# Performance work log

Hardware: AMD Instinct MI355X
Metric: run time of the kernel (lower is better)

The kernel has to match this reference:

```python
import jax, jax.numpy as jnp
import numpy as np

T, B_SZ = 1024, 1024
NX, NU, ND, NM, NDT, NH = 128, 64, 32, 32, 32, 128


def setup_inputs() -> dict:
    key = jax.random.key(0)
    ks = jax.random.split(key, 10)
    return {
        "x": jax.random.normal(ks[0], (B_SZ, NX), jnp.float32),
        "M_flow": jax.random.normal(ks[1], (T, B_SZ, NM), jnp.float32),
        "DT": jax.random.normal(ks[2], (T, B_SZ, NDT), jnp.float32),
        "D": jax.random.normal(ks[3], (T, B_SZ, ND), jnp.float32),
        # ConstrainedLinear(nx, nx): weight and scalar init with torch.rand -> uniform[0,1)
        "A_weight": jax.random.uniform(ks[4], (NX, NX), jnp.float32),
        "A_scalar": jax.random.uniform(ks[5], (NX, NX), jnp.float32),
        # nn.Linear(in, out, bias=False) weights are [out, in]
        "B_w": jax.random.normal(ks[6], (NX, NU), jnp.float32) * (1.0 / np.sqrt(NU)),
        "E_w": jax.random.normal(ks[7], (NX, ND), jnp.float32) * (1.0 / np.sqrt(ND)),
        "hf1_w": jax.random.normal(ks[8], (NH, NM + NDT), jnp.float32) * (1.0 / np.sqrt(NM + NDT)),
        "hf2_w": jax.random.normal(ks[9], (NU, NH), jnp.float32) * (1.0 / np.sqrt(NH)),
    }


def reference(x, M_flow, DT, D, A_weight, A_scalar, B_w, E_w, hf1_w, hf2_w):
    # Constrained weight: ((1 - 0.1*sigmoid(scalar)) * softmax(weight, dim=1)).T
    # It is constant across time, so compute once (torch redundantly recomputes it per step).
    s_clamped = 1.0 - 0.1 * jax.nn.sigmoid(A_scalar)
    W_eff = (s_clamped * jax.nn.softmax(A_weight, axis=1)).T  # [nx, nx]

    # Per-step control input u_t depends only on exogenous M_flow/DT -> vectorize over time.
    md = jnp.concatenate([M_flow, DT], axis=2)                # [T, B, n_m+n_dT]
    h = jax.nn.relu(jnp.einsum('tbi,hi->tbh', md, hf1_w))     # [T, B, n_hidden]
    u = jax.nn.relu(jnp.einsum('tbh,uh->tbu', h, hf2_w))      # [T, B, nu]

    # Precompute additive drive B(u_t) + E(d_t); only x@W_eff is sequential.
    drive = jnp.einsum('tbu,xu->tbx', u, B_w) + jnp.einsum('tbd,xd->tbx', D, E_w)

    def step(x_prev, drive_t):
        x_new = x_prev @ W_eff + drive_t
        return x_new, x_new

    _, X = jax.lax.scan(step, x, drive)  # X: [T, B, nx]
    Y = X[:, :, -1]                      # [T, B]
    return X, Y
```

## Files before the change

### kernel.cpp

```cpp
#include <hip/hip_runtime.h>

typedef _Float16 h4 __attribute__((ext_vector_type(4)));
typedef _Float16 h8 __attribute__((ext_vector_type(8)));
typedef float f4 __attribute__((ext_vector_type(4)));

#define MFMA16(a, b, c) __builtin_amdgcn_mfma_f32_16x16x32_f16((a), (b), (c), 0, 0, 0)

static constexpr int TT  = 1024;
static constexpr int BS  = 1024;
static constexpr int LCH = 64;
static constexpr int NCH = 16;
static constexpr size_t XTOT = (size_t)TT * BS * 128;

static constexpr size_t WS_WT16 = 0;
static constexpr size_t WS_HF1  = 32768;
static constexpr size_t WS_HF2  = 49152;
static constexpr size_t WS_BW   = 65536;
static constexpr size_t WS_EW   = 81920;
static constexpr size_t WS_WL16 = 90112;
static constexpr size_t WS_W32A = 122880;
static constexpr size_t WS_W32B = 188416;
static constexpr size_t WS_F    = 253952;
static constexpr size_t WS_INIT = WS_F + (size_t)16 * 1024 * 128 * 4;

__global__ void prep_kernel(const float* __restrict__ Aw, const float* __restrict__ As,
                            const float* __restrict__ hf1, const float* __restrict__ hf2,
                            const float* __restrict__ Bw, const float* __restrict__ Ew,
                            char* __restrict__ ws)
{
    const int tid = threadIdx.x;
    const int bid = blockIdx.x;
    if (bid < 128) {
        __shared__ float red[128];
        const int n = bid;
        const float a = Aw[n * 128 + tid];
        red[tid] = a;
        __syncthreads();
        for (int s = 64; s > 0; s >>= 1) {
            if (tid < s) red[tid] = fmaxf(red[tid], red[tid + s]);
            __syncthreads();
        }
        const float mx = red[0];
        __syncthreads();
        const float e = expf(a - mx);
        red[tid] = e;
        __syncthreads();
        for (int s = 64; s > 0; s >>= 1) {
            if (tid < s) red[tid] += red[tid + s];
            __syncthreads();
        }
        const float sm  = e / red[0];
        const float asv = As[n * 128 + tid];
        const float sc  = 1.0f - 0.1f * (1.0f / (1.0f + expf(-asv)));
        const float val = sc * sm;
        ((_Float16*)(ws + WS_WT16))[n * 128 + tid] = (_Float16)val;
        ((float*)(ws + WS_W32A))[n * 128 + tid]    = val;
    } else {
        const int b2 = bid - 128;
        for (int i = b2 * 128 + tid; i < 8192; i += 32 * 128) {
            ((_Float16*)(ws + WS_HF1))[i] = (_Float16)hf1[i];
            ((_Float16*)(ws + WS_HF2))[i] = (_Float16)hf2[i];
            ((_Float16*)(ws + WS_BW))[i]  = (_Float16)Bw[i];
            if (i < 4096) ((_Float16*)(ws + WS_EW))[i] = (_Float16)Ew[i];
        }
    }
}

__global__ void matsq_kernel(const float* __restrict__ in, float* __restrict__ out)
{
    const int idx = blockIdx.x * 256 + threadIdx.x;
    const int n = idx >> 7, k = idx & 127;
    float acc = 0.f;
    for (int m = 0; m < 128; ++m) acc += in[m * 128 + k] * in[n * 128 + m];
    out[idx] = acc;
}

__global__ void conv_kernel(const float* __restrict__ in, char* __restrict__ ws)
{
    const int idx = blockIdx.x * 256 + threadIdx.x;
    ((_Float16*)(ws + WS_WL16))[idx] = (_Float16)in[idx];
}

template <bool FINAL>
__global__ __launch_bounds__(256, 2)
void scan_chunk(const float* __restrict__ Mfl, const float* __restrict__ DTi,
                const float* __restrict__ Din, char* __restrict__ ws,
                float* __restrict__ Xout, float* __restrict__ Yout)
{
    const int tid  = threadIdx.x;
    const int lane = tid & 63;
    const int w    = tid >> 6;
    const int cl   = lane & 15;
    const int gq   = lane >> 4;
    const int bt   = blockIdx.x & 63;
    const int c    = blockIdx.x >> 6;
    const int b0   = bt * 16;

    const _Float16* Wt16 = (const _Float16*)(ws + WS_WT16);
    const _Float16* Hf1  = (const _Float16*)(ws + WS_HF1);
    const _Float16* Hf2  = (const _Float16*)(ws + WS_HF2);
    const _Float16* Bw16 = (const _Float16*)(ws + WS_BW);
    const _Float16* Ew16 = (const _Float16*)(ws + WS_EW);
    float* Fbuf          = (float*)(ws + WS_F);
    const float* Init    = (const float*)(ws + WS_INIT);

    __shared__ __align__(16) _Float16 xs[2][16 * 128];
    __shared__ __align__(16) _Float16 mds[16 * 64];
    __shared__ __align__(16) _Float16 hs[16 * 128];
    __shared__ __align__(16) _Float16 us[16 * 64];
    __shared__ __align__(16) _Float16 dts[16 * 32];

    h8 wtf[2][4], hf1f[2][2], bwf[2][2], ewf[2], hf2f[4];
#pragma unroll
    for (int nt = 0; nt < 2; ++nt) {
        const int ng = w * 32 + nt * 16 + cl;
#pragma unroll
        for (int kk = 0; kk < 4; ++kk)
            wtf[nt][kk] = *(const h8*)&Wt16[ng * 128 + kk * 32 + gq * 8];
#pragma unroll
        for (int kk = 0; kk < 2; ++kk) {
            hf1f[nt][kk] = *(const h8*)&Hf1[ng * 64 + kk * 32 + gq * 8];
            bwf[nt][kk]  = *(const h8*)&Bw16[ng * 64 + kk * 32 + gq * 8];
        }
        ewf[nt] = *(const h8*)&Ew16[ng * 32 + gq * 8];
    }
    {
        const int ng = w * 16 + cl;
#pragma unroll
        for (int kk = 0; kk < 4; ++kk)
            hf2f[kk] = *(const h8*)&Hf2[ng * 128 + kk * 32 + gq * 8];
    }

    if constexpr (FINAL) {
        const int row = tid >> 4, c8 = tid & 15;
        const float* src = &Init[((size_t)c * BS + b0 + row) * 128 + c8 * 8];
        f4 v0 = *(const f4*)src;
        f4 v1 = *(const f4*)(src + 4);
        h8 hv;
#pragma unroll
        for (int j = 0; j < 4; ++j) { hv[j] = (_Float16)v0[j]; hv[4 + j] = (_Float16)v1[j]; }
        *(h8*)&xs[0][row * 128 + ((c8 ^ row) & 15) * 8] = hv;
    } else {
        h8 z = {};
        *(h8*)&xs[0][tid * 8] = z;
    }

    f4 p0, p1;
    const int qrow = (tid & 127) >> 3;
    const int qc4  = (tid & 7) * 4;
    auto loadin = [&](int k) {
        const size_t t  = (size_t)c * LCH + k;
        const size_t rb = (t * BS + b0 + qrow) * 32 + qc4;
        p0 = (tid < 128) ? *(const f4*)&Mfl[rb] : *(const f4*)&DTi[rb];
        if (tid < 128) p1 = *(const f4*)&Din[rb];
    };
    loadin(0);

    int cur = 0;
    for (int k = 0; k < LCH; ++k) {
        {
            const int col = (tid < 128) ? qc4 : (32 + qc4);
            h4 hv;
#pragma unroll
            for (int j = 0; j < 4; ++j) hv[j] = (_Float16)p0[j];
            *(h4*)&mds[qrow * 64 + (((col >> 3) ^ (qrow & 7)) * 8) + (col & 7)] = hv;
            if (tid < 128) {
                h4 h2;
#pragma unroll
                for (int j = 0; j < 4; ++j) h2[j] = (_Float16)p1[j];
                *(h4*)&dts[qrow * 32 + (((qc4 >> 3) ^ (qrow & 3)) * 8) + (qc4 & 7)] = h2;
            }
        }
        if (k + 1 < LCH) loadin(k + 1);
        __syncthreads();

        f4 hacc[2] = {};
#pragma unroll
        for (int kk = 0; kk < 2; ++kk) {
            h8 a = *(const h8*)&mds[cl * 64 + (((kk * 4 + gq) ^ (cl & 7)) * 8)];
            hacc[0] = MFMA16(a, hf1f[0][kk], hacc[0]);
            hacc[1] = MFMA16(a, hf1f[1][kk], hacc[1]);
        }
#pragma unroll
        for (int nt = 0; nt < 2; ++nt) {
            const int colg = w * 32 + nt * 16 + cl;
#pragma unroll
            for (int r = 0; r < 4; ++r) {
                const int row = gq * 4 + r;
                hs[row * 128 + (((colg >> 3) ^ (row & 15)) * 8) + (colg & 7)] =
                    (_Float16)fmaxf(hacc[nt][r], 0.f);
            }
        }
        __syncthreads();

        f4 uacc = {};
#pragma unroll
        for (int kk = 0; kk < 4; ++kk) {
            h8 a = *(const h8*)&hs[cl * 128 + (((kk * 4 + gq) ^ (cl & 15)) * 8)];
            uacc = MFMA16(a, hf2f[kk], uacc);
        }
        {
            const int colg = w * 16 + cl;
#pragma unroll
            for (int r = 0; r < 4; ++r) {
                const int row = gq * 4 + r;
                us[row * 64 + (((colg >> 3) ^ (row & 7)) * 8) + (colg & 7)] =
                    (_Float16)fmaxf(uacc[r], 0.f);
            }
        }
        __syncthreads();

        f4 acc[2] = {};
#pragma unroll
        for (int kk = 0; kk < 2; ++kk) {
            h8 a = *(const h8*)&us[cl * 64 + (((kk * 4 + gq) ^ (cl & 7)) * 8)];
            acc[0] = MFMA16(a, bwf[0][kk], acc[0]);
            acc[1] = MFMA16(a, bwf[1][kk], acc[1]);
        }
        {
            h8 a = *(const h8*)&dts[cl * 32 + ((gq ^ (cl & 3)) * 8)];
            acc[0] = MFMA16(a, ewf[0], acc[0]);
            acc[1] = MFMA16(a, ewf[1], acc[1]);
        }
#pragma unroll
        for (int kk = 0; kk < 4; ++kk) {
            h8 a = *(const h8*)&xs[cur][cl * 128 + (((kk * 4 + gq) ^ (cl & 15)) * 8)];
            acc[0] = MFMA16(a, wtf[0][kk], acc[0]);
            acc[1] = MFMA16(a, wtf[1][kk], acc[1]);
        }

        const int nxt = cur ^ 1;
        if constexpr (FINAL) {
            const size_t t = (size_t)c * LCH + k;
#pragma unroll
            for (int nt = 0; nt < 2; ++nt) {
                const int colg = w * 32 + nt * 16 + cl;
#pragma unroll
                for (int r = 0; r < 4; ++r) {
                    const int row = gq * 4 + r;
                    const float v = acc[nt][r];
                    Xout[(t * BS + b0 + row) * 128 + colg] = v;
                    xs[nxt][row * 128 + (((colg >> 3) ^ (row & 15)) * 8) + (colg & 7)] =
                        (_Float16)v;
                }
            }
            if (w == 3 && cl == 15) {
#pragma unroll
                for (int r = 0; r < 4; ++r)
                    Yout[t * BS + b0 + gq * 4 + r] = acc[1][r];
            }
        } else {
            if (k == LCH - 1) {
#pragma unroll
                for (int nt = 0; nt < 2; ++nt) {
                    const int colg = w * 32 + nt * 16 + cl;
#pragma unroll
                    for (int r = 0; r < 4; ++r) {
                        const int row = gq * 4 + r;
                        Fbuf[((size_t)c * BS + b0 + row) * 128 + colg] = acc[nt][r];
                    }
                }
            } else {
#pragma unroll
                for (int nt = 0; nt < 2; ++nt) {
                    const int colg = w * 32 + nt * 16 + cl;
#pragma unroll
                    for (int r = 0; r < 4; ++r) {
                        const int row = gq * 4 + r;
                        xs[nxt][row * 128 + (((colg >> 3) ^ (row & 15)) * 8) + (colg & 7)] =
                            (_Float16)acc[nt][r];
                    }
                }
            }
        }
        cur = nxt;
    }
}

__global__ __launch_bounds__(256, 2)
void carry_kernel(const float* __restrict__ x_in, char* __restrict__ ws)
{
    const int tid  = threadIdx.x;
    const int lane = tid & 63;
    const int w    = tid >> 6;
    const int cl   = lane & 15;
    const int gq   = lane >> 4;
    const int b0   = blockIdx.x * 16;

    const _Float16* WL = (const _Float16*)(ws + WS_WL16);
    const float* Fbuf  = (const float*)(ws + WS_F);
    float* Init        = (float*)(ws + WS_INIT);

    __shared__ __align__(16) _Float16 xs[2][16 * 128];

    h8 wlf[2][4];
#pragma unroll
    for (int nt = 0; nt < 2; ++nt) {
        const int ng = w * 32 + nt * 16 + cl;
#pragma unroll
        for (int kk = 0; kk < 4; ++kk)
            wlf[nt][kk] = *(const h8*)&WL[ng * 128 + kk * 32 + gq * 8];
    }

    {
        const int row = tid >> 4, c8 = tid & 15;
        const float* src = &x_in[(b0 + row) * 128 + c8 * 8];
        f4 v0 = *(const f4*)src, v1 = *(const f4*)(src + 4);
        float* dst = &Init[((size_t)(b0 + row)) * 128 + c8 * 8];
        *(f4*)dst = v0;
        *(f4*)(dst + 4) = v1;
        h8 hv;
#pragma unroll
        for (int j = 0; j < 4; ++j) { hv[j] = (_Float16)v0[j]; hv[4 + j] = (_Float16)v1[j]; }
        *(h8*)&xs[0][row * 128 + ((c8 ^ row) & 15) * 8] = hv;
    }
    __syncthreads();

    int cur = 0;
    for (int cc = 1; cc < NCH; ++cc) {
        f4 acc[2] = {};
#pragma unroll
        for (int kk = 0; kk < 4; ++kk) {
            h8 a = *(const h8*)&xs[cur][cl * 128 + (((kk * 4 + gq) ^ (cl & 15)) * 8)];
            acc[0] = MFMA16(a, wlf[0][kk], acc[0]);
            acc[1] = MFMA16(a, wlf[1][kk], acc[1]);
        }
        const int nxt = cur ^ 1;
#pragma unroll
        for (int nt = 0; nt < 2; ++nt) {
            const int colg = w * 32 + nt * 16 + cl;
#pragma unroll
            for (int r = 0; r < 4; ++r) {
                const int row = gq * 4 + r;
                const float v =
                    acc[nt][r] + Fbuf[((size_t)(cc - 1) * BS + b0 + row) * 128 + colg];
                Init[((size_t)cc * BS + b0 + row) * 128 + colg] = v;
                xs[nxt][row * 128 + (((colg >> 3) ^ (row & 15)) * 8) + (colg & 7)] =
                    (_Float16)v;
            }
        }
        __syncthreads();
        cur = nxt;
    }
}

extern "C" void kernel_launch(void* const* d_in, const int* in_sizes, int n_in,
                              void* d_out, int out_size, void* d_ws, size_t ws_size,
                              hipStream_t stream)
{
    const float* x_in = (const float*)d_in[0];
    const float* Mfl  = (const float*)d_in[1];
    const float* DTi  = (const float*)d_in[2];
    const float* Din  = (const float*)d_in[3];
    const float* Aw   = (const float*)d_in[4];
    const float* As   = (const float*)d_in[5];
    const float* Bw   = (const float*)d_in[6];
    const float* Ew   = (const float*)d_in[7];
    const float* hf1  = (const float*)d_in[8];
    const float* hf2  = (const float*)d_in[9];
    char* ws   = (char*)d_ws;
    float* Xout = (float*)d_out;
    float* Yout = Xout + XTOT;

    prep_kernel<<<dim3(160), dim3(128), 0, stream>>>(Aw, As, hf1, hf2, Bw, Ew, ws);

    float* A32 = (float*)(ws + WS_W32A);
    float* B32 = (float*)(ws + WS_W32B);
    for (int i = 0; i < 6; ++i) {
        const float* src = (i & 1) ? B32 : A32;
        float* dst       = (i & 1) ? A32 : B32;
        matsq_kernel<<<dim3(64), dim3(256), 0, stream>>>(src, dst);
    }
    conv_kernel<<<dim3(64), dim3(256), 0, stream>>>(A32, ws);

    scan_chunk<false><<<dim3(15 * 64), dim3(256), 0, stream>>>(Mfl, DTi, Din, ws, nullptr, nullptr);
    carry_kernel<<<dim3(64), dim3(256), 0, stream>>>(x_in, ws);
    scan_chunk<true><<<dim3(16 * 64), dim3(256), 0, stream>>>(Mfl, DTi, Din, ws, Xout, Yout);
}
```

Before: 470.4 us.

## Precompute drive term in separate parallel kernel instead of recomputing in both scans

The MLP (hf1, hf2) plus the B/E projections were computed inside both scan passes, once for the local pass and again for the final pass. They are now computed once by a fully parallel drive_kernel that writes an fp16 drive buffer in the accumulator fragment layout. The scan kernels then only load one h8 per step, prefetched one step ahead, and do the x@W recurrence, which allows higher occupancy. This costs an extra fp16 buffer written and read twice, and it drops the W^64 conversion kernel by converting inside the carry kernel.

Measured after the change: 457.5 us. 2.7% less time.

```diff
diff --git a/kernel.cpp b/kernel.cpp
--- a/kernel.cpp
+++ b/kernel.cpp
@@ -17,11 +17,11 @@
 static constexpr size_t WS_HF2  = 49152;
 static constexpr size_t WS_BW   = 65536;
 static constexpr size_t WS_EW   = 81920;
-static constexpr size_t WS_WL16 = 90112;
 static constexpr size_t WS_W32A = 122880;
 static constexpr size_t WS_W32B = 188416;
 static constexpr size_t WS_F    = 253952;
-static constexpr size_t WS_INIT = WS_F + (size_t)16 * 1024 * 128 * 4;
+static constexpr size_t WS_INIT = WS_F + (size_t)NCH * BS * 128 * 4;
+static constexpr size_t WS_DRV  = WS_INIT + (size_t)NCH * BS * 128 * 4;
 
 __global__ void prep_kernel(const float* __restrict__ Aw, const float* __restrict__ As,
                             const float* __restrict__ hf1, const float* __restrict__ hf2,
@@ -75,17 +75,141 @@
     out[idx] = acc;
 }
 
-__global__ void conv_kernel(const float* __restrict__ in, char* __restrict__ ws)
-{
-    const int idx = blockIdx.x * 256 + threadIdx.x;
-    ((_Float16*)(ws + WS_WL16))[idx] = (_Float16)in[idx];
+__global__ __launch_bounds__(256, 3)
+void drive_kernel(const float* __restrict__ Mfl, const float* __restrict__ DTi,
+                  const float* __restrict__ Din, char* __restrict__ ws)
+{
+    const int tid  = threadIdx.x;
+    const int lane = tid & 63;
+    const int w    = tid >> 6;
+    const int cl   = lane & 15;
+    const int gq   = lane >> 4;
+    const int bt   = blockIdx.x & 63;
+    const int tq   = blockIdx.x >> 6;
+    const int b0   = bt * 16;
+
+    const _Float16* Hf1  = (const _Float16*)(ws + WS_HF1);
+    const _Float16* Hf2  = (const _Float16*)(ws + WS_HF2);
+    const _Float16* Bw16 = (const _Float16*)(ws + WS_BW);
+    const _Float16* Ew16 = (const _Float16*)(ws + WS_EW);
+    _Float16* Drv        = (_Float16*)(ws + WS_DRV);
+
+    __shared__ __align__(16) _Float16 mds[4][16 * 64];
+    __shared__ __align__(16) _Float16 dts[4][16 * 32];
+    __shared__ __align__(16) _Float16 hs[4][16 * 128];
+    __shared__ __align__(16) _Float16 us[4][16 * 64];
+
+    h8 hf1f[2][2], bwf[2][2], ewf[2], hf2f[4];
+#pragma unroll
+    for (int nt = 0; nt < 2; ++nt) {
+        const int ng = w * 32 + nt * 16 + cl;
+#pragma unroll
+        for (int kk = 0; kk < 2; ++kk) {
+            hf1f[nt][kk] = *(const h8*)&Hf1[ng * 64 + kk * 32 + gq * 8];
+            bwf[nt][kk]  = *(const h8*)&Bw16[ng * 64 + kk * 32 + gq * 8];
+        }
+        ewf[nt] = *(const h8*)&Ew16[ng * 32 + gq * 8];
+    }
+    {
+        const int ng = w * 16 + cl;
+#pragma unroll
+        for (int kk = 0; kk < 4; ++kk)
+            hf2f[kk] = *(const h8*)&Hf2[ng * 128 + kk * 32 + gq * 8];
+    }
+
+    const int qrow = (tid & 127) >> 3;
+    const int qc4  = (tid & 7) * 4;
+    f4 pm[4], pd[4];
+#pragma unroll
+    for (int s = 0; s < 4; ++s) {
+        const size_t t  = (size_t)tq * 4 + s;
+        const size_t rb = (t * BS + b0 + qrow) * 32 + qc4;
+        pm[s] = (tid < 128) ? *(const f4*)&Mfl[rb] : *(const f4*)&DTi[rb];
+        if (tid < 128) pd[s] = *(const f4*)&Din[rb];
+    }
+#pragma unroll
+    for (int s = 0; s < 4; ++s) {
+        const int col = (tid < 128) ? qc4 : (32 + qc4);
+        h4 hv;
+#pragma unroll
+        for (int j = 0; j < 4; ++j) hv[j] = (_Float16)pm[s][j];
+        *(h4*)&mds[s][qrow * 64 + (((col >> 3) ^ (qrow & 7)) * 8) + (col & 7)] = hv;
+        if (tid < 128) {
+            h4 h2;
+#pragma unroll
+            for (int j = 0; j < 4; ++j) h2[j] = (_Float16)pd[s][j];
+            *(h4*)&dts[s][qrow * 32 + (((qc4 >> 3) ^ (qrow & 3)) * 8) + (qc4 & 7)] = h2;
+        }
+    }
+    __syncthreads();
+
+#pragma unroll
+    for (int s = 0; s < 4; ++s) {
+        f4 ha[2] = {};
+#pragma unroll
+        for (int kk = 0; kk < 2; ++kk) {
+            h8 a = *(const h8*)&mds[s][cl * 64 + (((kk * 4 + gq) ^ (cl & 7)) * 8)];
+            ha[0] = MFMA16(a, hf1f[0][kk], ha[0]);
+            ha[1] = MFMA16(a, hf1f[1][kk], ha[1]);
+        }
+#pragma unroll
+        for (int nt = 0; nt < 2; ++nt) {
+            const int colg = w * 32 + nt * 16 + cl;
+#pragma unroll
+            for (int r = 0; r < 4; ++r) {
+                const int row = gq * 4 + r;
+                hs[s][row * 128 + (((colg >> 3) ^ (row & 15)) * 8) + (colg & 7)] =
+                    (_Float16)fmaxf(ha[nt][r], 0.f);
+            }
+        }
+    }
+    __syncthreads();
+
+#pragma unroll
+    for (int s = 0; s < 4; ++s) {
+        f4 ua = {};
+#pragma unroll
+        for (int kk = 0; kk < 4; ++kk) {
+            h8 a = *(const h8*)&hs[s][cl * 128 + (((kk * 4 + gq) ^ (cl & 15)) * 8)];
+            ua = MFMA16(a, hf2f[kk], ua);
+        }
+        const int colg = w * 16 + cl;
+#pragma unroll
+        for (int r = 0; r < 4; ++r) {
+            const int row = gq * 4 + r;
+            us[s][row * 64 + (((colg >> 3) ^ (row & 7)) * 8) + (colg & 7)] =
+                (_Float16)fmaxf(ua[r], 0.f);
+        }
+    }
+    __syncthreads();
+
+#pragma unroll
+    for (int s = 0; s < 4; ++s) {
+        f4 acc[2] = {};
+#pragma unroll
+        for (int kk = 0; kk < 2; ++kk) {
+            h8 a = *(const h8*)&us[s][cl * 64 + (((kk * 4 + gq) ^ (cl & 7)) * 8)];
+            acc[0] = MFMA16(a, bwf[0][kk], acc[0]);
+            acc[1] = MFMA16(a, bwf[1][kk], acc[1]);
+        }
+        {
+            h8 a = *(const h8*)&dts[s][cl * 32 + ((gq ^ (cl & 3)) * 8)];
+            acc[0] = MFMA16(a, ewf[0], acc[0]);
+            acc[1] = MFMA16(a, ewf[1], acc[1]);
+        }
+        h8 hv;
+#pragma unroll
+        for (int nt = 0; nt < 2; ++nt)
+#pragma unroll
+            for (int r = 0; r < 4; ++r) hv[nt * 4 + r] = (_Float16)acc[nt][r];
+        const size_t t = (size_t)tq * 4 + s;
+        *(h8*)&Drv[((t * 64 + bt) * 256 + tid) * 8] = hv;
+    }
 }
 
 template <bool FINAL>
-__global__ __launch_bounds__(256, 2)
-void scan_chunk(const float* __restrict__ Mfl, const float* __restrict__ DTi,
-                const float* __restrict__ Din, char* __restrict__ ws,
-                float* __restrict__ Xout, float* __restrict__ Yout)
+__global__ __launch_bounds__(256, 4)
+void scan_kernel(char* __restrict__ ws, float* __restrict__ Xout, float* __restrict__ Yout)
 {
     const int tid  = threadIdx.x;
     const int lane = tid & 63;
@@ -97,38 +221,19 @@
     const int b0   = bt * 16;
 
     const _Float16* Wt16 = (const _Float16*)(ws + WS_WT16);
-    const _Float16* Hf1  = (const _Float16*)(ws + WS_HF1);
-    const _Float16* Hf2  = (const _Float16*)(ws + WS_HF2);
-    const _Float16* Bw16 = (const _Float16*)(ws + WS_BW);
-    const _Float16* Ew16 = (const _Float16*)(ws + WS_EW);
+    const _Float16* Drv  = (const _Float16*)(ws + WS_DRV);
     float* Fbuf          = (float*)(ws + WS_F);
     const float* Init    = (const float*)(ws + WS_INIT);
 
     __shared__ __align__(16) _Float16 xs[2][16 * 128];
-    __shared__ __align__(16) _Float16 mds[16 * 64];
-    __shared__ __align__(16) _Float16 hs[16 * 128];
-    __shared__ __align__(16) _Float16 us[16 * 64];
-    __shared__ __align__(16) _Float16 dts[16 * 32];
-
-    h8 wtf[2][4], hf1f[2][2], bwf[2][2], ewf[2], hf2f[4];
+
+    h8 wtf[2][4];
 #pragma unroll
     for (int nt = 0; nt < 2; ++nt) {
         const int ng = w * 32 + nt * 16 + cl;
 #pragma unroll
         for (int kk = 0; kk < 4; ++kk)
             wtf[nt][kk] = *(const h8*)&Wt16[ng * 128 + kk * 32 + gq * 8];
-#pragma unroll
-        for (int kk = 0; kk < 2; ++kk) {
-            hf1f[nt][kk] = *(const h8*)&Hf1[ng * 64 + kk * 32 + gq * 8];
-            bwf[nt][kk]  = *(const h8*)&Bw16[ng * 64 + kk * 32 + gq * 8];
-        }
-        ewf[nt] = *(const h8*)&Ew16[ng * 32 + gq * 8];
-    }
-    {
-        const int ng = w * 16 + cl;
-#pragma unroll
-        for (int kk = 0; kk < 4; ++kk)
-            hf2f[kk] = *(const h8*)&Hf2[ng * 128 + kk * 32 + gq * 8];
     }
 
     if constexpr (FINAL) {
@@ -144,84 +249,21 @@
         h8 z = {};
         *(h8*)&xs[0][tid * 8] = z;
     }
-
-    f4 p0, p1;
-    const int qrow = (tid & 127) >> 3;
-    const int qc4  = (tid & 7) * 4;
-    auto loadin = [&](int k) {
-        const size_t t  = (size_t)c * LCH + k;
-        const size_t rb = (t * BS + b0 + qrow) * 32 + qc4;
-        p0 = (tid < 128) ? *(const f4*)&Mfl[rb] : *(const f4*)&DTi[rb];
-        if (tid < 128) p1 = *(const f4*)&Din[rb];
-    };
-    loadin(0);
+    __syncthreads();
+
+    const size_t dbase = (((size_t)c * 64) * 64 + bt) * 2048 + (size_t)tid * 8;
+    h8 dc = *(const h8*)&Drv[dbase];
 
     int cur = 0;
     for (int k = 0; k < LCH; ++k) {
-        {
-            const int col = (tid < 128) ? qc4 : (32 + qc4);
-            h4 hv;
-#pragma unroll
-            for (int j = 0; j < 4; ++j) hv[j] = (_Float16)p0[j];
-            *(h4*)&mds[qrow * 64 + (((col >> 3) ^ (qrow & 7)) * 8) + (col & 7)] = hv;
-            if (tid < 128) {
-                h4 h2;
-#pragma unroll
-                for (int j = 0; j < 4; ++j) h2[j] = (_Float16)p1[j];
-                *(h4*)&dts[qrow * 32 + (((qc4 >> 3) ^ (qrow & 3)) * 8) + (qc4 & 7)] = h2;
-            }
-        }
-        if (k + 1 < LCH) loadin(k + 1);
-        __syncthreads();
-
-        f4 hacc[2] = {};
-#pragma unroll
-        for (int kk = 0; kk < 2; ++kk) {
-            h8 a = *(const h8*)&mds[cl * 64 + (((kk * 4 + gq) ^ (cl & 7)) * 8)];
-            hacc[0] = MFMA16(a, hf1f[0][kk], hacc[0]);
-            hacc[1] = MFMA16(a, hf1f[1][kk], hacc[1]);
-        }
-#pragma unroll
-        for (int nt = 0; nt < 2; ++nt) {
-            const int colg = w * 32 + nt * 16 + cl;
-#pragma unroll
-            for (int r = 0; r < 4; ++r) {
-                const int row = gq * 4 + r;
-                hs[row * 128 + (((colg >> 3) ^ (row & 15)) * 8) + (colg & 7)] =
-                    (_Float16)fmaxf(hacc[nt][r], 0.f);
-            }
-        }
-        __syncthreads();
-
-        f4 uacc = {};
-#pragma unroll
-        for (int kk = 0; kk < 4; ++kk) {
-            h8 a = *(const h8*)&hs[cl * 128 + (((kk * 4 + gq) ^ (cl & 15)) * 8)];
-            uacc = MFMA16(a, hf2f[kk], uacc);
-        }
-        {
-            const int colg = w * 16 + cl;
-#pragma unroll
-            for (int r = 0; r < 4; ++r) {
-                const int row = gq * 4 + r;
-                us[row * 64 + (((colg >> 3) ^ (row & 7)) * 8) + (colg & 7)] =
-                    (_Float16)fmaxf(uacc[r], 0.f);
-            }
-        }
-        __syncthreads();
-
-        f4 acc[2] = {};
-#pragma unroll
-        for (int kk = 0; kk < 2; ++kk) {
-            h8 a = *(const h8*)&us[cl * 64 + (((kk * 4 + gq) ^ (cl & 7)) * 8)];
-            acc[0] = MFMA16(a, bwf[0][kk], acc[0]);
-            acc[1] = MFMA16(a, bwf[1][kk], acc[1]);
-        }
-        {
-            h8 a = *(const h8*)&dts[cl * 32 + ((gq ^ (cl & 3)) * 8)];
-            acc[0] = MFMA16(a, ewf[0], acc[0]);
-            acc[1] = MFMA16(a, ewf[1], acc[1]);
-        }
+        f4 acc[2];
+#pragma unroll
+        for (int nt = 0; nt < 2; ++nt)
+#pragma unroll
+            for (int r = 0; r < 4; ++r) acc[nt][r] = (float)dc[nt * 4 + r];
+
+        if (k + 1 < LCH) dc = *(const h8*)&Drv[dbase + (size_t)(k + 1) * 64 * 2048];
+
 #pragma unroll
         for (int kk = 0; kk < 4; ++kk) {
             h8 a = *(const h8*)&xs[cur][cl * 128 + (((kk * 4 + gq) ^ (cl & 15)) * 8)];
@@ -273,6 +315,7 @@
                 }
             }
         }
+        __syncthreads();
         cur = nxt;
     }
 }
@@ -287,9 +330,9 @@
     const int gq   = lane >> 4;
     const int b0   = blockIdx.x * 16;
 
-    const _Float16* WL = (const _Float16*)(ws + WS_WL16);
-    const float* Fbuf  = (const float*)(ws + WS_F);
-    float* Init        = (float*)(ws + WS_INIT);
+    const float* WL32 = (const float*)(ws + WS_W32A);
+    const float* Fbuf = (const float*)(ws + WS_F);
+    float* Init       = (float*)(ws + WS_INIT);
 
     __shared__ __align__(16) _Float16 xs[2][16 * 128];
 
@@ -298,8 +341,15 @@
     for (int nt = 0; nt < 2; ++nt) {
         const int ng = w * 32 + nt * 16 + cl;
 #pragma unroll
-        for (int kk = 0; kk < 4; ++kk)
-            wlf[nt][kk] = *(const h8*)&WL[ng * 128 + kk * 32 + gq * 8];
+        for (int kk = 0; kk < 4; ++kk) {
+            f4 a0 = *(const f4*)&WL32[ng * 128 + kk * 32 + gq * 8];
+            f4 a1 = *(const f4*)&WL32[ng * 128 + kk * 32 + gq * 8 + 4];
+#pragma unroll
+            for (int j = 0; j < 4; ++j) {
+                wlf[nt][kk][j]     = (_Float16)a0[j];
+                wlf[nt][kk][4 + j] = (_Float16)a1[j];
+            }
+        }
     }
 
     {
@@ -358,7 +408,7 @@
     const float* Ew   = (const float*)d_in[7];
     const float* hf1  = (const float*)d_in[8];
     const float* hf2  = (const float*)d_in[9];
-    char* ws   = (char*)d_ws;
+    char* ws    = (char*)d_ws;
     float* Xout = (float*)d_out;
     float* Yout = Xout + XTOT;
 
@@ -371,9 +421,10 @@
         float* dst       = (i & 1) ? A32 : B32;
         matsq_kernel<<<dim3(64), dim3(256), 0, stream>>>(src, dst);
     }
-    conv_kernel<<<dim3(64), dim3(256), 0, stream>>>(A32, ws);
-
-    scan_chunk<false><<<dim3(15 * 64), dim3(256), 0, stream>>>(Mfl, DTi, Din, ws, nullptr, nullptr);
+
+    drive_kernel<<<dim3(256 * 64), dim3(256), 0, stream>>>(Mfl, DTi, Din, ws);
+
+    scan_kernel<false><<<dim3(15 * 64), dim3(256), 0, stream>>>(ws, nullptr, nullptr);
     carry_kernel<<<dim3(64), dim3(256), 0, stream>>>(x_in, ws);
-    scan_chunk<true><<<dim3(16 * 64), dim3(256), 0, stream>>>(Mfl, DTi, Din, ws, Xout, Yout);
-}
+    scan_kernel<true><<<dim3(16 * 64), dim3(256), 0, stream>>>(ws, Xout, Yout);
+}
```
